# Kernel optimization log

Measured on AMD Instinct MI355X. Metric: run time of the kernel, lower is better.

Reference implementation:

```python
import jax, jax.numpy as jnp
import numpy as np

EPS = 1e-10  # faithful quirk: masked scores are set to eps, NOT -inf
LN_EPS = 1e-5
N_HEADS, D_MODEL, D_HEAD, D_MLP = 16, 1024, 64, 4096
INIT_RANGE = 0.02


def setup_inputs() -> dict:
    key = jax.random.key(0)
    ks = jax.random.split(key, 8)
    B, S = 2, 2048
    inp = {
        'residual': jax.random.normal(ks[0], (B, S, D_MODEL), jnp.float32),
        'W_key': jax.random.normal(ks[1], (N_HEADS, D_MODEL, D_HEAD), jnp.float32) * INIT_RANGE,
        'W_query': jax.random.normal(ks[2], (N_HEADS, D_MODEL, D_HEAD), jnp.float32) * INIT_RANGE,
        'W_values': jax.random.normal(ks[3], (N_HEADS, D_MODEL, D_HEAD), jnp.float32) * INIT_RANGE,
        'W_attn_out': jax.random.normal(ks[4], (N_HEADS, D_HEAD, D_MODEL), jnp.float32) * INIT_RANGE,
        'B_key': jnp.zeros((N_HEADS, D_HEAD), jnp.float32),
        'B_query': jnp.zeros((N_HEADS, D_HEAD), jnp.float32),
        'B_values': jnp.zeros((N_HEADS, D_HEAD), jnp.float32),
        'B_attn_out': jnp.zeros((D_MODEL,), jnp.float32),
        'ln1_w': jnp.ones((D_MODEL,), jnp.float32),
        'ln1_b': jnp.zeros((D_MODEL,), jnp.float32),
        'ln2_w': jnp.ones((D_MODEL,), jnp.float32),
        'ln2_b': jnp.zeros((D_MODEL,), jnp.float32),
        'W_mlp_in': jax.random.normal(ks[5], (D_MODEL, D_MLP), jnp.float32) * INIT_RANGE,
        'W_mlp_out': jax.random.normal(ks[6], (D_MLP, D_MODEL), jnp.float32) * INIT_RANGE,
        'B_mlp_in': jnp.zeros((D_MLP,), jnp.float32),
        'B_mlp_out': jnp.zeros((D_MODEL,), jnp.float32),
    }
    return inp


def _layernorm(x, w, b):
    mean = jnp.mean(x, axis=-1, keepdims=True)
    var = jnp.mean(jnp.square(x - mean), axis=-1, keepdims=True)  # biased var
    return (x - mean) / jnp.sqrt(var + LN_EPS) * w + b


def _attention(x, W_key, W_query, W_values, W_attn_out,
               B_key, B_query, B_values, B_attn_out):
    S = x.shape[1]
    keys = jnp.einsum('bse,neh->bsnh', x, W_key) + B_key
    queries = jnp.einsum('bse,neh->bsnh', x, W_query) + B_query
    values = jnp.einsum('bse,neh->bsnh', x, W_values) + B_values
    scores = jnp.einsum('bknh,bqnh->bnqk', keys, queries) / (D_HEAD ** 0.5)
    # faithful to source: positions where query < key are set to eps (not -inf)
    q_idx = jnp.arange(S)[:, None]
    k_idx = jnp.arange(S)[None, :]
    scores = jnp.where(q_idx < k_idx, EPS, scores)
    probs = jax.nn.softmax(scores, axis=3)
    weighted = jnp.einsum('bnqk,bknh->bqnh', probs, values)
    out = jnp.einsum('bqnh,nhe->bqe', weighted, W_attn_out) + B_attn_out
    return out


def reference(residual, W_key, W_query, W_values, W_attn_out,
              B_key, B_query, B_values, B_attn_out,
              ln1_w, ln1_b, ln2_w, ln2_b,
              W_mlp_in, W_mlp_out, B_mlp_in, B_mlp_out):
    mid = _attention(_layernorm(residual, ln1_w, ln1_b),
                     W_key, W_query, W_values, W_attn_out,
                     B_key, B_query, B_values, B_attn_out) + residual
    h = jnp.einsum('bse,em->bsm', _layernorm(mid, ln2_w, ln2_b), W_mlp_in) + B_mlp_in
    h = jax.nn.gelu(h, approximate=False)  # torch nn.GELU default = exact erf
    out = jnp.einsum('bsm,me->bse', h, W_mlp_out) + B_mlp_out + mid
    return out
```

## Files before the change

kernel.cpp:

```cpp
#include <hip/hip_runtime.h>
#include <hip/hip_bf16.h>


typedef __hip_bfloat16 bf16;
typedef __bf16 bf16x8 __attribute__((ext_vector_type(8)));
typedef float f32x4 __attribute__((ext_vector_type(4)));
typedef unsigned short u16x8 __attribute__((ext_vector_type(8)));
#define DEV static __device__ __forceinline__

DEV float b2f(bf16 v) { return __bfloat162float(v); }
DEV bf16 f2b(float v) { return __float2bfloat16(v); }
DEV unsigned short f2bu(float v) { return __builtin_bit_cast(unsigned short, __float2bfloat16(v)); }
DEV float ldin(const void* p, size_t i, int f32) {
  return f32 ? ((const float*)p)[i] : b2f(((const bf16*)p)[i]);
}
DEV void stout(void* p, size_t i, int f32, float v) {
  if (f32) ((float*)p)[i] = v;
  else     ((bf16*)p)[i] = f2b(v);
}
DEV f32x4 mfma16(bf16x8 a, bf16x8 b, f32x4 c) {
  return __builtin_amdgcn_mfma_f32_16x16x32_bf16(a, b, c, 0, 0, 0);
}
DEV float exp2fast(float x) {
  float r;
  asm volatile("v_exp_f32 %0, %1\n\ts_nop 0" : "=v"(r) : "v"(x));
  return r;
}
DEV void gload16(const void* g, void* l) {
  __builtin_amdgcn_global_load_lds(
      (const __attribute__((address_space(1))) unsigned int*)g,
      (__attribute__((address_space(3))) unsigned int*)l, 16, 0, 0);
}

__global__ void detect_kernel(const void* __restrict__ ln1w, int* __restrict__ flag) {
  if (threadIdx.x == 0 && blockIdx.x == 0) {
    const unsigned short* u = (const unsigned short*)ln1w;
    flag[0] = (u[0] == 0x3F80u) ? 0 : 1;
  }
}

__global__ void pack_bias(const void* __restrict__ Bq, const void* __restrict__ Bk,
                          const void* __restrict__ Bv, const void* __restrict__ Bao,
                          const void* __restrict__ Bmi, const void* __restrict__ Bmo,
                          const int* __restrict__ flagp, float* __restrict__ out) {
  int t = blockIdx.x * 256 + threadIdx.x;
  if (t >= 9216) return;
  int f32 = flagp[0];
  float v;
  if (t < 1024)      v = ldin(Bq, t, f32);
  else if (t < 2048) v = ldin(Bk, t - 1024, f32);
  else if (t < 3072) v = ldin(Bv, t - 2048, f32);
  else if (t < 4096) v = ldin(Bao, t - 3072, f32);
  else if (t < 8192) v = ldin(Bmi, t - 4096, f32);
  else               v = ldin(Bmo, t - 8192, f32);
  out[t] = v;
}

__global__ __launch_bounds__(256) void tsplit(const void* __restrict__ src,
                                              bf16* __restrict__ hi,
                                              const int* __restrict__ flagp,
                                              int K, int N) {
  int i = blockIdx.x * 256 + threadIdx.x;
  int f32 = flagp[0];
  int k = i / N, n = i - k * N;
  float v = ldin(src, i, f32);
  hi[(size_t)n * K + k] = f2b(v);
}

__global__ __launch_bounds__(256) void tsplit_qkv(const void* __restrict__ Wq,
                                                  const void* __restrict__ Wk,
                                                  const void* __restrict__ Wv,
                                                  bf16* __restrict__ hi,
                                                  const int* __restrict__ flagp) {
  int i = blockIdx.x * 256 + threadIdx.x;
  int f32 = flagp[0];
  int sec = i >> 20;
  int rem = i & 1048575;
  int hh = rem >> 16, kr = rem & 65535;
  int k = kr >> 6, d = kr & 63;
  const void* W = (sec == 0) ? Wq : (sec == 1) ? Wk : Wv;
  float v = ldin(W, (size_t)hh * 65536 + (size_t)k * 64 + d, f32);
  int n = sec * 1024 + hh * 64 + d;
  hi[(size_t)n * 1024 + k] = f2b(v);
}

__global__ __launch_bounds__(256) void vsuffix(const bf16* __restrict__ v2,
                                               float* __restrict__ suf) {
  const int head = blockIdx.x >> 6, d = blockIdx.x & 63;
  const int t = threadIdx.x;
  const int T = t >> 3, s0 = (t & 7) * 8;
  const bf16* src = v2 + (size_t)head * 131072 + (size_t)T * 4096 + d * 64 + s0;
  u16x8 u = *(const u16x8*)src;
  float s = 0.f;
#pragma unroll
  for (int j = 0; j < 8; j++) s += b2f(__builtin_bit_cast(bf16, (unsigned short)u[j]));
#pragma unroll
  for (int off = 1; off < 8; off <<= 1) s += __shfl_xor(s, off);
  __shared__ float cs[32];
  if ((t & 7) == 0) cs[T] = s;
  __syncthreads();
  if (t < 33) {
    float acc = 0.f;
    for (int j = t; j < 32; j++) acc += cs[j];
    suf[((size_t)head * 33 + t) * 64 + d] = acc;
  }
}

__global__ __launch_bounds__(256) void ln_kernel(const void* __restrict__ x,
                                                 const void* __restrict__ w,
                                                 const void* __restrict__ bb,
                                                 bf16* __restrict__ out,
                                                 const int* __restrict__ flagp) {
  const int f32 = flagp[0];
  const int row = blockIdx.x, t = threadIdx.x;
  const size_t base = (size_t)row * 1024;
  float v[4];
#pragma unroll
  for (int i = 0; i < 4; i++) v[i] = ldin(x, base + t + 256 * i, f32);
  float s1 = v[0] + v[1] + v[2] + v[3];
  float s2 = v[0] * v[0] + v[1] * v[1] + v[2] * v[2] + v[3] * v[3];
#pragma unroll
  for (int off = 32; off; off >>= 1) {
    s1 += __shfl_xor(s1, off);
    s2 += __shfl_xor(s2, off);
  }
  __shared__ float r1[4], r2[4];
  if ((t & 63) == 0) { r1[t >> 6] = s1; r2[t >> 6] = s2; }
  __syncthreads();
  s1 = r1[0] + r1[1] + r1[2] + r1[3];
  s2 = r2[0] + r2[1] + r2[2] + r2[3];
  float mean = s1 * (1.f / 1024.f);
  float var = s2 * (1.f / 1024.f) - mean * mean;
  float rstd = rsqrtf(var + 1e-5f);
#pragma unroll
  for (int i = 0; i < 4; i++) {
    int idx = t + 256 * i;
    out[base + idx] = f2b((v[i] - mean) * rstd * ldin(w, idx, f32) + ldin(bb, idx, f32));
  }
}

template <int MODE>
__global__ __launch_bounds__(256) void gemm_bt2(const bf16* __restrict__ A,
                                                const bf16* __restrict__ BT,
                                                const float* __restrict__ bias,
                                                const void* extra, void* outp,
                                                const int* __restrict__ flagp,
                                                int N, int K) {
  __shared__ __align__(16) unsigned short As[128][64];
  __shared__ __align__(16) unsigned short Bs[128][64];
  const int f32 = flagp[0];
  const int t = threadIdx.x;
  const int lane = t & 63, wv = t >> 6;
  const int quad = lane >> 4, l15 = lane & 15;
  const int wm = (wv >> 1) * 64, wn = (wv & 1) * 64;
  const int m0 = blockIdx.y * 128, n0 = blockIdx.x * 128;
  f32x4 acc[4][4] = {};
  const int rl = lane >> 3, G = lane & 7;
  const int sg = (G ^ rl) * 8;
  const int l7 = l15 & 7;
  for (int k0 = 0; k0 < K; k0 += 64) {
#pragma unroll
    for (int c = 0; c < 4; c++) {
      const int ch = wv * 4 + c;
      const int row = ch * 8 + rl;
      gload16(A + (size_t)(m0 + row) * K + k0 + sg, &As[ch * 8][0]);
      gload16(BT + (size_t)(n0 + row) * K + k0 + sg, &Bs[ch * 8][0]);
    }
    __syncthreads();
#pragma unroll
    for (int sub = 0; sub < 2; sub++) {
      const int gsw = (((sub * 4 + quad) ^ l7)) * 8;
      bf16x8 af[4], bh[4];
#pragma unroll
      for (int f = 0; f < 4; f++) {
        af[f] = __builtin_bit_cast(bf16x8, *(const u16x8*)&As[wm + f * 16 + l15][gsw]);
        bh[f] = __builtin_bit_cast(bf16x8, *(const u16x8*)&Bs[wn + f * 16 + l15][gsw]);
      }
#pragma unroll
      for (int fm = 0; fm < 4; fm++)
#pragma unroll
        for (int fn = 0; fn < 4; fn++)
          acc[fm][fn] = mfma16(af[fm], bh[fn], acc[fm][fn]);
    }
    __syncthreads();
  }
  if (MODE == 3) {
    bf16* q2 = (bf16*)outp;
    bf16* k2 = q2 + 4194304;
    bf16* v2 = (bf16*)const_cast<void*>(extra);
#pragma unroll
    for (int fm = 0; fm < 4; fm++) {
      int rowb = m0 + wm + fm * 16 + quad * 4;
      int bq = rowb >> 11, sb = rowb & 2047;
#pragma unroll
      for (int fn = 0; fn < 4; fn++) {
        int col = n0 + wn + fn * 16 + l15;
        float bcol = bias[col];
        int sec = col >> 10;
        int hd = col & 1023;
        size_t hbase = (size_t)(bq * 16 + (hd >> 6)) * 131072;
        int d = hd & 63;
        if (sec == 2) {
          unsigned long long pk = 0;
#pragma unroll
          for (int r = 0; r < 4; r++)
            pk |= (unsigned long long)f2bu(acc[fm][fn][r] + bcol) << (16 * r);
          *(unsigned long long*)&v2[hbase + (size_t)(sb >> 6) * 4096 + d * 64 + (sb & 63)] = pk;
        } else {
          bf16* dst = sec ? k2 : q2;
#pragma unroll
          for (int r = 0; r < 4; r++)
            dst[hbase + (size_t)(sb + r) * 64 + d] = f2b(acc[fm][fn][r] + bcol);
        }
      }
    }
  } else {
#pragma unroll
    for (int fm = 0; fm < 4; fm++) {
#pragma unroll
      for (int r = 0; r < 4; r++) {
        int row = m0 + wm + fm * 16 + quad * 4 + r;
#pragma unroll
        for (int fn = 0; fn < 4; fn++) {
          int col = n0 + wn + fn * 16 + l15;
          float v = acc[fm][fn][r] + bias[col];
          if (MODE == 1) {
            size_t idx = (size_t)row * N + col;
            v += ldin(extra, idx, f32);
            stout(outp, idx, f32, v);
          } else {
            v = 0.5f * v * (1.f + erff(v * 0.70710678118654752f));
            ((bf16*)outp)[(size_t)row * N + col] = f2b(v);
          }
        }
      }
    }
  }
}

__global__ __launch_bounds__(256) void gemm_bt3(const bf16* __restrict__ A,
                                                const bf16* __restrict__ BT,
                                                const float* __restrict__ bias,
                                                const void* extra, void* outp,
                                                const int* __restrict__ flagp,
                                                int N, int K) {
  __shared__ __align__(16) unsigned short As[64][64];
  __shared__ __align__(16) unsigned short Bs[128][64];
  const int f32 = flagp[0];
  const int t = threadIdx.x;
  const int lane = t & 63, wv = t >> 6;
  const int quad = lane >> 4, l15 = lane & 15;
  const int wm = (wv >> 1) * 32, wn = (wv & 1) * 64;
  const int m0 = blockIdx.y * 64, n0 = blockIdx.x * 128;
  f32x4 acc[2][4] = {};
  const int rl = lane >> 3, G = lane & 7;
  const int sg = (G ^ rl) * 8;
  const int l7 = l15 & 7;
  for (int k0 = 0; k0 < K; k0 += 64) {
#pragma unroll
    for (int c = 0; c < 2; c++) {
      const int ch = wv * 2 + c;
      gload16(A + (size_t)(m0 + ch * 8 + rl) * K + k0 + sg, &As[ch * 8][0]);
    }
#pragma unroll
    for (int c = 0; c < 4; c++) {
      const int ch = wv * 4 + c;
      gload16(BT + (size_t)(n0 + ch * 8 + rl) * K + k0 + sg, &Bs[ch * 8][0]);
    }
    __syncthreads();
#pragma unroll
    for (int sub = 0; sub < 2; sub++) {
      const int gsw = (((sub * 4 + quad) ^ l7)) * 8;
      bf16x8 af[2], bh[4];
#pragma unroll
      for (int f = 0; f < 2; f++)
        af[f] = __builtin_bit_cast(bf16x8, *(const u16x8*)&As[wm + f * 16 + l15][gsw]);
#pragma unroll
      for (int f = 0; f < 4; f++)
        bh[f] = __builtin_bit_cast(bf16x8, *(const u16x8*)&Bs[wn + f * 16 + l15][gsw]);
#pragma unroll
      for (int fm = 0; fm < 2; fm++)
#pragma unroll
        for (int fn = 0; fn < 4; fn++)
          acc[fm][fn] = mfma16(af[fm], bh[fn], acc[fm][fn]);
    }
    __syncthreads();
  }
#pragma unroll
  for (int fm = 0; fm < 2; fm++) {
#pragma unroll
    for (int r = 0; r < 4; r++) {
      int row = m0 + wm + fm * 16 + quad * 4 + r;
#pragma unroll
      for (int fn = 0; fn < 4; fn++) {
        int col = n0 + wn + fn * 16 + l15;
        float v = acc[fm][fn][r] + bias[col];
        size_t idx = (size_t)row * N + col;
        v += ldin(extra, idx, f32);
        stout(outp, idx, f32, v);
      }
    }
  }
}

template <int MODE, int QKV>
__global__ __launch_bounds__(256) void gemm_nn(const bf16* __restrict__ A,
                                               const void* __restrict__ B0,
                                               const void* __restrict__ B1,
                                               const void* __restrict__ B2,
                                               const float* __restrict__ bias,
                                               const void* extra, void* outp,
                                               const int* __restrict__ flagp,
                                               int N, int K, size_t ooff) {
  __shared__ unsigned short As[128][40];
  __shared__ unsigned short Bh[128][40];
  __shared__ unsigned short Bl[128][40];
  const int f32 = flagp[0];
  const int t = threadIdx.x;
  const int lane = t & 63, wv = t >> 6;
  const int quad = lane >> 4, l15 = lane & 15;
  const int wm = (wv >> 1) * 64, wn = (wv & 1) * 64;
  const int m0 = blockIdx.y * 128, n0 = blockIdx.x * 128;
  const void* B = B0;
  if (QKV) B = (n0 < 1024) ? B0 : (n0 < 2048) ? B1 : B2;
  f32x4 acc[4][4] = {};
  const int row_a = t >> 2;
  const int kc = (t & 3) * 8;
  const int cB = t & 127;
  const int e0 = t >> 7;
  for (int k0 = 0; k0 < K; k0 += 32) {
    uint4 a0 = *(const uint4*)(A + (size_t)(m0 + row_a) * K + k0 + kc);
    uint4 a1 = *(const uint4*)(A + (size_t)(m0 + 64 + row_a) * K + k0 + kc);
    *(uint4*)&As[row_a][kc] = a0;
    *(uint4*)&As[64 + row_a][kc] = a1;
#pragma unroll
    for (int rep = 0; rep < 8; rep++) {
      int e = (rep * 2 + e0) * 2;
      size_t a0i, a1i;
      if (QKV) {
        int cs = (n0 + cB) & 1023;
        size_t wb = (size_t)(cs >> 6) * 65536 + (cs & 63);
        a0i = wb + (size_t)(k0 + e) * 64;
        a1i = wb + (size_t)(k0 + e + 1) * 64;
      } else {
        a0i = (size_t)(k0 + e) * N + n0 + cB;
        a1i = a0i + N;
      }
      float v0 = ldin(B, a0i, f32);
      float v1 = ldin(B, a1i, f32);
      unsigned short h0 = f2bu(v0), h1 = f2bu(v1);
      float l0 = v0 - b2f(__builtin_bit_cast(bf16, h0));
      float l1 = v1 - b2f(__builtin_bit_cast(bf16, h1));
      *(unsigned int*)&Bh[cB][e] = (unsigned int)h0 | ((unsigned int)h1 << 16);
      *(unsigned int*)&Bl[cB][e] = (unsigned int)f2bu(l0) | ((unsigned int)f2bu(l1) << 16);
    }
    __syncthreads();
    bf16x8 af[4], bh[4], bl[4];
#pragma unroll
    for (int f = 0; f < 4; f++) {
      af[f] = __builtin_bit_cast(bf16x8, *(const u16x8*)&As[wm + f * 16 + l15][quad * 8]);
      bh[f] = __builtin_bit_cast(bf16x8, *(const u16x8*)&Bh[wn + f * 16 + l15][quad * 8]);
      bl[f] = __builtin_bit_cast(bf16x8, *(const u16x8*)&Bl[wn + f * 16 + l15][quad * 8]);
    }
#pragma unroll
    for (int fm = 0; fm < 4; fm++)
#pragma unroll
      for (int fn = 0; fn < 4; fn++)
        acc[fm][fn] = mfma16(af[fm], bh[fn], acc[fm][fn]);
    if (f32) {
#pragma unroll
      for (int fm = 0; fm < 4; fm++)
#pragma unroll
        for (int fn = 0; fn < 4; fn++)
          acc[fm][fn] = mfma16(af[fm], bl[fn], acc[fm][fn]);
    }
    __syncthreads();
  }
#pragma unroll
  for (int fm = 0; fm < 4; fm++) {
#pragma unroll
    for (int r = 0; r < 4; r++) {
      int row = m0 + wm + fm * 16 + quad * 4 + r;
#pragma unroll
      for (int fn = 0; fn < 4; fn++) {
        int col = n0 + wn + fn * 16 + l15;
        float v = acc[fm][fn][r] + bias[col];
        size_t idx = (size_t)row * N + col;
        if (MODE == 1) {
          v += ldin(extra, ooff + idx, f32);
          stout(outp, ooff + idx, f32, v);
        } else if (MODE == 2) {
          v = 0.5f * v * (1.f + erff(v * 0.70710678118654752f));
          ((bf16*)outp)[idx] = f2b(v);
        } else {
          ((bf16*)outp)[idx] = f2b(v);
        }
      }
    }
  }
}

__global__ __launch_bounds__(256) void attn_split(const bf16* __restrict__ qkv2,
                                                  const float* __restrict__ suf,
                                                  float* __restrict__ part0,
                                                  float* __restrict__ part1,
                                                  float* __restrict__ lp0buf,
                                                  float* __restrict__ lp1buf,
                                                  bf16* __restrict__ weighted) {
  __shared__ __align__(16) unsigned short P[2][4][16][72];
  const int t = threadIdx.x;
  const int lane = t & 63, wv = t >> 6;
  const int quad = lane >> 4, l15 = lane & 15;
  const int p = blockIdx.x;
  const int g = p & 31;
  const int wi = p >> 5;
  int qc, Tlo, Thi, mode;
  if (wi < 32) {
    qc = 31 - (wi >> 1);
    if ((wi & 1) == 0) { Tlo = 0; Thi = 15; mode = 1; }
    else               { Tlo = 16; Thi = qc; mode = 2; }
  } else {
    qc = 47 - wi; Tlo = 0; Thi = qc; mode = 0;
  }
  const int b = g >> 4, n = g & 15;
  const int q0 = qc * 64 + wv * 16;
  const bf16* Qh = qkv2 + (size_t)g * 131072;
  const bf16* Kh = qkv2 + 4194304 + (size_t)g * 131072;
  const bf16* Vh = qkv2 + 8388608 + (size_t)g * 131072;
  bf16x8 aq0, aq1;
  {
    u16x8 u0 = *(const u16x8*)(Qh + (size_t)(q0 + l15) * 64 + quad * 8);
    u16x8 u1 = *(const u16x8*)(Qh + (size_t)(q0 + l15) * 64 + 32 + quad * 8);
    aq0 = __builtin_bit_cast(bf16x8, u0);
    aq1 = __builtin_bit_cast(bf16x8, u1);
  }
  float lpA[4] = {0.f, 0.f, 0.f, 0.f}, lpB[4] = {0.f, 0.f, 0.f, 0.f};
  f32x4 oA[4] = {}, oB[4] = {};
  const float C = 0.125f * 1.44269504088896f;
  const int qgb = q0 + quad * 4;
  auto tile = [&](int T, int st, f32x4* o, float* lp) {
    const int kk = T * 64;
    const bf16* Vt = Vh + (size_t)T * 4096;
    u16x8 vu[2][4];
#pragma unroll
    for (int sl = 0; sl < 2; sl++)
#pragma unroll
      for (int f = 0; f < 4; f++)
        vu[sl][f] = *(const u16x8*)(Vt + (size_t)(f * 16 + l15) * 64 + sl * 32 + quad * 8);
    f32x4 s[4];
#pragma unroll
    for (int sub = 0; sub < 4; sub++) {
      int krow = kk + sub * 16 + l15;
      u16x8 uk0 = *(const u16x8*)(Kh + (size_t)krow * 64 + quad * 8);
      u16x8 uk1 = *(const u16x8*)(Kh + (size_t)krow * 64 + 32 + quad * 8);
      f32x4 sc = {0.f, 0.f, 0.f, 0.f};
      sc = mfma16(aq0, __builtin_bit_cast(bf16x8, uk0), sc);
      sc = mfma16(aq1, __builtin_bit_cast(bf16x8, uk1), sc);
      s[sub] = sc;
    }
#pragma unroll
    for (int sub = 0; sub < 4; sub++) {
#pragma unroll
      for (int r = 0; r < 4; r++) {
        float pv = exp2fast(s[sub][r] * C);
        int kg = kk + sub * 16 + l15;
        pv = (qgb + r < kg) ? 1.0f : pv;
        lp[r] += pv;
        P[st][wv][quad * 4 + r][l15 + 16 * sub] = f2bu(pv);
      }
    }
    u16x8 pu0 = *(const u16x8*)&P[st][wv][l15][quad * 8];
    u16x8 pu1 = *(const u16x8*)&P[st][wv][l15][32 + quad * 8];
#pragma unroll
    for (int f = 0; f < 4; f++) {
      o[f] = mfma16(__builtin_bit_cast(bf16x8, pu0), __builtin_bit_cast(bf16x8, vu[0][f]), o[f]);
      o[f] = mfma16(__builtin_bit_cast(bf16x8, pu1), __builtin_bit_cast(bf16x8, vu[1][f]), o[f]);
    }
  };
  int T = Tlo;
  for (; T + 1 <= Thi; T += 2) {
    tile(T, 0, oA, lpA);
    tile(T + 1, 1, oB, lpB);
  }
  if (T <= Thi) tile(T, 0, oA, lpA);
  float lp[4];
  f32x4 o[4];
#pragma unroll
  for (int r = 0; r < 4; r++) lp[r] = lpA[r] + lpB[r];
#pragma unroll
  for (int f = 0; f < 4; f++) o[f] = oA[f] + oB[f];
  if (mode != 1) {
    const float* sp = suf + ((size_t)g * 33 + (qc + 1)) * 64;
#pragma unroll
    for (int f = 0; f < 4; f++) {
      float sv = sp[f * 16 + l15];
#pragma unroll
      for (int r = 0; r < 4; r++) o[f][r] += sv;
    }
  }
#pragma unroll
  for (int off = 8; off; off >>= 1)
#pragma unroll
    for (int r = 0; r < 4; r++) lp[r] += __shfl_xor(lp[r], off);
  if (mode == 0) {
    const float mcnt = (float)(2048 - 64 * (qc + 1));
#pragma unroll
    for (int r = 0; r < 4; r++) {
      float inv = 1.f / (lp[r] + mcnt);
      int qg = q0 + quad * 4 + r;
      size_t base = (size_t)(b * 2048 + qg) * 1024 + n * 64;
#pragma unroll
      for (int f = 0; f < 4; f++)
        weighted[base + f * 16 + l15] = f2b(o[f][r] * inv);
    }
  } else {
    float* part = (mode == 1) ? part0 : part1;
    float* lpb  = (mode == 1) ? lp0buf : lp1buf;
    size_t pb = (size_t)(g * 16 + (qc - 16)) * 4096;
#pragma unroll
    for (int r = 0; r < 4; r++) {
      int row = wv * 16 + quad * 4 + r;
#pragma unroll
      for (int f = 0; f < 4; f++)
        part[pb + (size_t)row * 64 + f * 16 + l15] = o[f][r];
      if (l15 == 0) lpb[(size_t)(g * 16 + (qc - 16)) * 64 + row] = lp[r];
    }
  }
}

__global__ __launch_bounds__(256) void attn_combine(const float* __restrict__ part0,
                                                    const float* __restrict__ part1,
                                                    const float* __restrict__ lp0,
                                                    const float* __restrict__ lp1,
                                                    bf16* __restrict__ weighted) {
  int i = blockIdx.x * 256 + threadIdx.x;
  int d = i & 63, row = (i >> 6) & 63, qq = (i >> 12) & 15, g = i >> 16;
  int qc = qq + 16;
  size_t pi = ((size_t)(g * 16 + qq) * 64 + row) * 64 + d;
  float o = part0[pi] + part1[pi];
  size_t li = (size_t)(g * 16 + qq) * 64 + row;
  float mcnt = (float)(2048 - 64 * (qc + 1));
  float lp = lp0[li] + lp1[li] + mcnt;
  int b = g >> 4, n = g & 15;
  int qg = qc * 64 + row;
  weighted[(size_t)(b * 2048 + qg) * 1024 + n * 64 + d] = f2b(o / lp);
}

__global__ __launch_bounds__(256) void attn_old(const bf16* __restrict__ qkv,
                                                bf16* __restrict__ weighted) {
  __shared__ unsigned short P[4][16][40];
  const int t = threadIdx.x;
  const int lane = t & 63, wv = t >> 6;
  const int quad = lane >> 4, l15 = lane & 15;
  const int bid = blockIdx.x;
  const int qc = bid & 31, bn = bid >> 5;
  const int b = bn >> 4, n = bn & 15;
  const int q0 = qc * 64 + wv * 16;
  const bf16* Qb = qkv + (size_t)b * 2048 * 3072 + n * 64;
  const bf16* Kb = Qb + 1024;
  const unsigned short* Vus = (const unsigned short*)(Qb + 2048);
  bf16x8 aq0, aq1;
  {
    u16x8 u0 = *(const u16x8*)(Qb + (size_t)(q0 + l15) * 3072 + quad * 8);
    u16x8 u1 = *(const u16x8*)(Qb + (size_t)(q0 + l15) * 3072 + 32 + quad * 8);
    aq0 = __builtin_bit_cast(bf16x8, u0);
    aq1 = __builtin_bit_cast(bf16x8, u1);
  }
  float m_[4] = {-30000.f, -30000.f, -30000.f, -30000.f};
  float l_[4] = {0.f, 0.f, 0.f, 0.f};
  f32x4 o[4] = {};
  for (int kk = 0; kk < 2048; kk += 32) {
    f32x4 s[2];
#pragma unroll
    for (int sub = 0; sub < 2; sub++) {
      int krow = kk + sub * 16 + l15;
      u16x8 uk0 = *(const u16x8*)(Kb + (size_t)krow * 3072 + quad * 8);
      u16x8 uk1 = *(const u16x8*)(Kb + (size_t)krow * 3072 + 32 + quad * 8);
      f32x4 sc = {0.f, 0.f, 0.f, 0.f};
      sc = mfma16(aq0, __builtin_bit_cast(bf16x8, uk0), sc);
      sc = mfma16(aq1, __builtin_bit_cast(bf16x8, uk1), sc);
#pragma unroll
      for (int r = 0; r < 4; r++) {
        int qg = q0 + quad * 4 + r;
        int kg = kk + sub * 16 + l15;
        s[sub][r] = (qg < kg) ? 1e-10f : sc[r] * 0.125f;
      }
    }
    float mr[4];
#pragma unroll
    for (int r = 0; r < 4; r++) mr[r] = fmaxf(s[0][r], s[1][r]);
#pragma unroll
    for (int off = 8; off; off >>= 1)
#pragma unroll
      for (int r = 0; r < 4; r++) mr[r] = fmaxf(mr[r], __shfl_xor(mr[r], off));
    float al[4];
#pragma unroll
    for (int r = 0; r < 4; r++) {
      float mn = fmaxf(m_[r], mr[r]);
      al[r] = __expf(m_[r] - mn);
      m_[r] = mn;
    }
    f32x4 p0, p1;
    float rs[4];
#pragma unroll
    for (int r = 0; r < 4; r++) {
      p0[r] = __expf(s[0][r] - m_[r]);
      p1[r] = __expf(s[1][r] - m_[r]);
      rs[r] = p0[r] + p1[r];
    }
#pragma unroll
    for (int off = 8; off; off >>= 1)
#pragma unroll
      for (int r = 0; r < 4; r++) rs[r] += __shfl_xor(rs[r], off);
#pragma unroll
    for (int r = 0; r < 4; r++) l_[r] = l_[r] * al[r] + rs[r];
#pragma unroll
    for (int f = 0; f < 4; f++)
#pragma unroll
      for (int r = 0; r < 4; r++) o[f][r] *= al[r];
#pragma unroll
    for (int r = 0; r < 4; r++) {
      P[wv][quad * 4 + r][l15] = f2bu(p0[r]);
      P[wv][quad * 4 + r][16 + l15] = f2bu(p1[r]);
    }
    __syncthreads();
    u16x8 pu = *(const u16x8*)&P[wv][l15][quad * 8];
    bf16x8 pf = __builtin_bit_cast(bf16x8, pu);
#pragma unroll
    for (int f = 0; f < 4; f++) {
      u16x8 vu;
#pragma unroll
      for (int j = 0; j < 8; j++)
        vu[j] = Vus[(size_t)(kk + quad * 8 + j) * 3072 + f * 16 + l15];
      o[f] = mfma16(pf, __builtin_bit_cast(bf16x8, vu), o[f]);
    }
    __syncthreads();
  }
#pragma unroll
  for (int r = 0; r < 4; r++) {
    float inv = 1.f / l_[r];
    int qg = q0 + quad * 4 + r;
    size_t base = (size_t)(b * 2048 + qg) * 1024 + n * 64;
#pragma unroll
    for (int f = 0; f < 4; f++)
      weighted[base + f * 16 + l15] = f2b(o[f][r] * inv);
  }
}

extern "C" void kernel_launch(void* const* d_in, const int* in_sizes, int n_in,
                              void* d_out, int out_size, void* d_ws, size_t ws_size,
                              hipStream_t stream) {
  const void* residual = d_in[0];
  const void* W_key    = d_in[1];
  const void* W_query  = d_in[2];
  const void* W_values = d_in[3];
  const void* W_ao     = d_in[4];
  const void* B_key    = d_in[5];
  const void* B_query  = d_in[6];
  const void* B_values = d_in[7];
  const void* B_ao     = d_in[8];
  const void* ln1w     = d_in[9];
  const void* ln1b     = d_in[10];
  const void* ln2w     = d_in[11];
  const void* ln2b     = d_in[12];
  const void* W_mi     = d_in[13];
  const void* W_mo     = d_in[14];
  const void* B_mi     = d_in[15];
  const void* B_mo     = d_in[16];

  char* ws = (char*)d_ws;
  float* biasA  = (float*)ws;
  int*   flag   = (int*)(ws + 36864);
  bf16*  slotA  = (bf16*)(ws + 40960);
  bf16*  xn = slotA, *wtd = slotA, *xn2 = slotA;

  detect_kernel<<<1, 64, 0, stream>>>(ln1w, flag);
  pack_bias<<<36, 256, 0, stream>>>(B_query, B_key, B_values, B_ao, B_mi, B_mo,
                                    flag, biasA);

  if (ws_size >= (size_t)83927040) {
    bf16*  qkv2    = (bf16*)(ws + 8429568);
    bf16*  q2      = qkv2;
    bf16*  v2      = qkv2 + 8388608;
    bf16*  h       = (bf16*)(ws + 8429568);
    bf16*  qkvT_hi = (bf16*)(ws + 33595392);
    float* suf     = (float*)(ws + 39886848);
    float* lp0buf  = (float*)(ws + 40157184);
    float* lp1buf  = (float*)(ws + 40288256);
    bf16*  aoT_hi  = (bf16*)(ws + 46178304);
    bf16*  miT_hi  = (bf16*)(ws + 50372608);
    float* part0   = (float*)(ws + 58761216);
    bf16*  moT_hi  = (bf16*)(ws + 67149824);
    float* part1   = (float*)(ws + 75538432);

    tsplit_qkv<<<12288, 256, 0, stream>>>(W_query, W_key, W_values, qkvT_hi, flag);
    tsplit<<<4096, 256, 0, stream>>>(W_ao, aoT_hi, flag, 1024, 1024);
    tsplit<<<16384, 256, 0, stream>>>(W_mi, miT_hi, flag, 1024, 4096);
    tsplit<<<16384, 256, 0, stream>>>(W_mo, moT_hi, flag, 4096, 1024);

    ln_kernel<<<4096, 256, 0, stream>>>(residual, ln1w, ln1b, xn, flag);
    gemm_bt2<3><<<dim3(24, 32), 256, 0, stream>>>(xn, qkvT_hi, biasA,
                                                  v2, q2, flag, 3072, 1024);
    vsuffix<<<2048, 256, 0, stream>>>(v2, suf);
    attn_split<<<1536, 256, 0, stream>>>(qkv2, suf, part0, part1,
                                         lp0buf, lp1buf, wtd);
    attn_combine<<<8192, 256, 0, stream>>>(part0, part1, lp0buf, lp1buf, wtd);
    gemm_bt3<<<dim3(8, 64), 256, 0, stream>>>(wtd, aoT_hi, biasA + 3072,
                                              residual, d_out, flag, 1024, 1024);
    ln_kernel<<<4096, 256, 0, stream>>>(d_out, ln2w, ln2b, xn2, flag);
    gemm_bt2<2><<<dim3(32, 32), 256, 0, stream>>>(xn2, miT_hi, biasA + 4096,
                                                  nullptr, h, flag, 4096, 1024);
    gemm_bt3<<<dim3(8, 64), 256, 0, stream>>>(h, moT_hi, biasA + 8192,
                                              d_out, d_out, flag, 1024, 4096);
  } else {
    bf16* qkv   = (bf16*)(ws + 8429568);
    bf16* hhalf = (bf16*)(ws + 16818176);

    ln_kernel<<<4096, 256, 0, stream>>>(residual, ln1w, ln1b, xn, flag);
    gemm_nn<0, 1><<<dim3(24, 32), 256, 0, stream>>>(xn, W_query, W_key, W_values,
                                                    biasA, nullptr, qkv, flag,
                                                    3072, 1024, 0);
    attn_old<<<1024, 256, 0, stream>>>(qkv, wtd);
    gemm_nn<1, 0><<<dim3(8, 32), 256, 0, stream>>>(wtd, W_ao, nullptr, nullptr,
                                                   biasA + 3072, residual, d_out,
                                                   flag, 1024, 1024, 0);
    ln_kernel<<<4096, 256, 0, stream>>>(d_out, ln2w, ln2b, xn2, flag);
    for (int half = 0; half < 2; ++half) {
      const bf16* a2 = xn2 + (size_t)half * 2048 * 1024;
      size_t ooff = (size_t)half * 2048 * 1024;
      gemm_nn<2, 0><<<dim3(32, 16), 256, 0, stream>>>(a2, W_mi, nullptr, nullptr,
                                                      biasA + 4096, nullptr, hhalf,
                                                      flag, 4096, 1024, 0);
      gemm_nn<1, 0><<<dim3(8, 16), 256, 0, stream>>>(hhalf, W_mo, nullptr, nullptr,
                                                     biasA + 8192, d_out, d_out,
                                                     flag, 1024, 4096, ooff);
    }
  }
}
```

Measured before the change: 543.0 us.

## Give each attention wave a full 64-query chunk to reuse K/V loads

Each wavefront now handles all four 16-row query groups of a 64-query work item, where before the four waves of a block shared one item with 16 rows each. Every K/V tile a wave loads is reused across 64 queries, cutting redundant global and L2 traffic by roughly four times. The grid shrinks from 1536 to 384 blocks, and the even/odd double accumulators are dropped. The cost is many more live registers per wave (64 accumulator floats plus Q fragments), with launch_bounds(256,2) set to hold occupancy, and the total number of waves available to spread load imbalance falls.

```diff
diff --git a/kernel.cpp b/kernel.cpp
--- a/kernel.cpp
+++ b/kernel.cpp
@@ -400,20 +400,20 @@
   }
 }
 
-__global__ __launch_bounds__(256) void attn_split(const bf16* __restrict__ qkv2,
-                                                  const float* __restrict__ suf,
-                                                  float* __restrict__ part0,
-                                                  float* __restrict__ part1,
-                                                  float* __restrict__ lp0buf,
-                                                  float* __restrict__ lp1buf,
-                                                  bf16* __restrict__ weighted) {
-  __shared__ __align__(16) unsigned short P[2][4][16][72];
+__global__ __launch_bounds__(256, 2) void attn_split(const bf16* __restrict__ qkv2,
+                                                     const float* __restrict__ suf,
+                                                     float* __restrict__ part0,
+                                                     float* __restrict__ part1,
+                                                     float* __restrict__ lp0buf,
+                                                     float* __restrict__ lp1buf,
+                                                     bf16* __restrict__ weighted) {
+  __shared__ __align__(16) unsigned short P[4][4][16][72];
   const int t = threadIdx.x;
   const int lane = t & 63, wv = t >> 6;
   const int quad = lane >> 4, l15 = lane & 15;
-  const int p = blockIdx.x;
-  const int g = p & 31;
-  const int wi = p >> 5;
+  const int w = blockIdx.x * 4 + wv;
+  const int g = w & 31;
+  const int wi = w >> 5;
   int qc, Tlo, Thi, mode;
   if (wi < 32) {
     qc = 31 - (wi >> 1);
@@ -423,23 +423,28 @@
     qc = 47 - wi; Tlo = 0; Thi = qc; mode = 0;
   }
   const int b = g >> 4, n = g & 15;
-  const int q0 = qc * 64 + wv * 16;
   const bf16* Qh = qkv2 + (size_t)g * 131072;
   const bf16* Kh = qkv2 + 4194304 + (size_t)g * 131072;
   const bf16* Vh = qkv2 + 8388608 + (size_t)g * 131072;
-  bf16x8 aq0, aq1;
-  {
-    u16x8 u0 = *(const u16x8*)(Qh + (size_t)(q0 + l15) * 64 + quad * 8);
-    u16x8 u1 = *(const u16x8*)(Qh + (size_t)(q0 + l15) * 64 + 32 + quad * 8);
-    aq0 = __builtin_bit_cast(bf16x8, u0);
-    aq1 = __builtin_bit_cast(bf16x8, u1);
-  }
-  float lpA[4] = {0.f, 0.f, 0.f, 0.f}, lpB[4] = {0.f, 0.f, 0.f, 0.f};
-  f32x4 oA[4] = {}, oB[4] = {};
+  bf16x8 aq[4][2];
+#pragma unroll
+  for (int qg = 0; qg < 4; qg++) {
+    size_t qr = (size_t)(qc * 64 + qg * 16 + l15) * 64;
+    aq[qg][0] = __builtin_bit_cast(bf16x8, *(const u16x8*)(Qh + qr + quad * 8));
+    aq[qg][1] = __builtin_bit_cast(bf16x8, *(const u16x8*)(Qh + qr + 32 + quad * 8));
+  }
+  float lp[4][4] = {};
+  f32x4 o[4][4] = {};
   const float C = 0.125f * 1.44269504088896f;
-  const int qgb = q0 + quad * 4;
-  auto tile = [&](int T, int st, f32x4* o, float* lp) {
+  for (int T = Tlo; T <= Thi; ++T) {
     const int kk = T * 64;
+    u16x8 uk[4][2];
+#pragma unroll
+    for (int sub = 0; sub < 4; sub++) {
+      size_t kr = (size_t)(kk + sub * 16 + l15) * 64;
+      uk[sub][0] = *(const u16x8*)(Kh + kr + quad * 8);
+      uk[sub][1] = *(const u16x8*)(Kh + kr + 32 + quad * 8);
+    }
     const bf16* Vt = Vh + (size_t)T * 4096;
     u16x8 vu[2][4];
 #pragma unroll
@@ -447,83 +452,82 @@
 #pragma unroll
       for (int f = 0; f < 4; f++)
         vu[sl][f] = *(const u16x8*)(Vt + (size_t)(f * 16 + l15) * 64 + sl * 32 + quad * 8);
-    f32x4 s[4];
-#pragma unroll
-    for (int sub = 0; sub < 4; sub++) {
-      int krow = kk + sub * 16 + l15;
-      u16x8 uk0 = *(const u16x8*)(Kh + (size_t)krow * 64 + quad * 8);
-      u16x8 uk1 = *(const u16x8*)(Kh + (size_t)krow * 64 + 32 + quad * 8);
-      f32x4 sc = {0.f, 0.f, 0.f, 0.f};
-      sc = mfma16(aq0, __builtin_bit_cast(bf16x8, uk0), sc);
-      sc = mfma16(aq1, __builtin_bit_cast(bf16x8, uk1), sc);
-      s[sub] = sc;
-    }
-#pragma unroll
-    for (int sub = 0; sub < 4; sub++) {
-#pragma unroll
-      for (int r = 0; r < 4; r++) {
-        float pv = exp2fast(s[sub][r] * C);
-        int kg = kk + sub * 16 + l15;
-        pv = (qgb + r < kg) ? 1.0f : pv;
-        lp[r] += pv;
-        P[st][wv][quad * 4 + r][l15 + 16 * sub] = f2bu(pv);
-      }
-    }
-    u16x8 pu0 = *(const u16x8*)&P[st][wv][l15][quad * 8];
-    u16x8 pu1 = *(const u16x8*)&P[st][wv][l15][32 + quad * 8];
-#pragma unroll
-    for (int f = 0; f < 4; f++) {
-      o[f] = mfma16(__builtin_bit_cast(bf16x8, pu0), __builtin_bit_cast(bf16x8, vu[0][f]), o[f]);
-      o[f] = mfma16(__builtin_bit_cast(bf16x8, pu1), __builtin_bit_cast(bf16x8, vu[1][f]), o[f]);
-    }
-  };
-  int T = Tlo;
-  for (; T + 1 <= Thi; T += 2) {
-    tile(T, 0, oA, lpA);
-    tile(T + 1, 1, oB, lpB);
-  }
-  if (T <= Thi) tile(T, 0, oA, lpA);
-  float lp[4];
-  f32x4 o[4];
-#pragma unroll
-  for (int r = 0; r < 4; r++) lp[r] = lpA[r] + lpB[r];
-#pragma unroll
-  for (int f = 0; f < 4; f++) o[f] = oA[f] + oB[f];
+#pragma unroll
+    for (int qg = 0; qg < 4; qg++) {
+      const int qgb = qc * 64 + qg * 16 + quad * 4;
+      f32x4 s[4];
+#pragma unroll
+      for (int sub = 0; sub < 4; sub++) {
+        f32x4 sc = {0.f, 0.f, 0.f, 0.f};
+        sc = mfma16(aq[qg][0], __builtin_bit_cast(bf16x8, uk[sub][0]), sc);
+        sc = mfma16(aq[qg][1], __builtin_bit_cast(bf16x8, uk[sub][1]), sc);
+        s[sub] = sc;
+      }
+#pragma unroll
+      for (int sub = 0; sub < 4; sub++) {
+#pragma unroll
+        for (int r = 0; r < 4; r++) {
+          float pv = exp2fast(s[sub][r] * C);
+          int kg = kk + sub * 16 + l15;
+          pv = (qgb + r < kg) ? 1.0f : pv;
+          lp[qg][r] += pv;
+          P[wv][qg][quad * 4 + r][l15 + 16 * sub] = f2bu(pv);
+        }
+      }
+      u16x8 pu0 = *(const u16x8*)&P[wv][qg][l15][quad * 8];
+      u16x8 pu1 = *(const u16x8*)&P[wv][qg][l15][32 + quad * 8];
+#pragma unroll
+      for (int f = 0; f < 4; f++) {
+        o[qg][f] = mfma16(__builtin_bit_cast(bf16x8, pu0), __builtin_bit_cast(bf16x8, vu[0][f]), o[qg][f]);
+        o[qg][f] = mfma16(__builtin_bit_cast(bf16x8, pu1), __builtin_bit_cast(bf16x8, vu[1][f]), o[qg][f]);
+      }
+    }
+  }
   if (mode != 1) {
     const float* sp = suf + ((size_t)g * 33 + (qc + 1)) * 64;
 #pragma unroll
     for (int f = 0; f < 4; f++) {
       float sv = sp[f * 16 + l15];
 #pragma unroll
-      for (int r = 0; r < 4; r++) o[f][r] += sv;
+      for (int qg = 0; qg < 4; qg++)
+#pragma unroll
+        for (int r = 0; r < 4; r++) o[qg][f][r] += sv;
     }
   }
 #pragma unroll
   for (int off = 8; off; off >>= 1)
 #pragma unroll
-    for (int r = 0; r < 4; r++) lp[r] += __shfl_xor(lp[r], off);
+    for (int qg = 0; qg < 4; qg++)
+#pragma unroll
+      for (int r = 0; r < 4; r++) lp[qg][r] += __shfl_xor(lp[qg][r], off);
   if (mode == 0) {
     const float mcnt = (float)(2048 - 64 * (qc + 1));
 #pragma unroll
-    for (int r = 0; r < 4; r++) {
-      float inv = 1.f / (lp[r] + mcnt);
-      int qg = q0 + quad * 4 + r;
-      size_t base = (size_t)(b * 2048 + qg) * 1024 + n * 64;
-#pragma unroll
-      for (int f = 0; f < 4; f++)
-        weighted[base + f * 16 + l15] = f2b(o[f][r] * inv);
+    for (int qg = 0; qg < 4; qg++) {
+#pragma unroll
+      for (int r = 0; r < 4; r++) {
+        float inv = 1.f / (lp[qg][r] + mcnt);
+        int qg_row = qc * 64 + qg * 16 + quad * 4 + r;
+        size_t base = (size_t)(b * 2048 + qg_row) * 1024 + n * 64;
+#pragma unroll
+        for (int f = 0; f < 4; f++)
+          weighted[base + f * 16 + l15] = f2b(o[qg][f][r] * inv);
+      }
     }
   } else {
     float* part = (mode == 1) ? part0 : part1;
     float* lpb  = (mode == 1) ? lp0buf : lp1buf;
     size_t pb = (size_t)(g * 16 + (qc - 16)) * 4096;
 #pragma unroll
-    for (int r = 0; r < 4; r++) {
-      int row = wv * 16 + quad * 4 + r;
-#pragma unroll
-      for (int f = 0; f < 4; f++)
-        part[pb + (size_t)row * 64 + f * 16 + l15] = o[f][r];
-      if (l15 == 0) lpb[(size_t)(g * 16 + (qc - 16)) * 64 + row] = lp[r];
+    for (int qg = 0; qg < 4; qg++) {
+#pragma unroll
+      for (int r = 0; r < 4; r++) {
+        int row = qg * 16 + quad * 4 + r;
+#pragma unroll
+        for (int f = 0; f < 4; f++)
+          part[pb + (size_t)row * 64 + f * 16 + l15] = o[qg][f][r];
+        if (l15 == 0) lpb[(size_t)(g * 16 + (qc - 16)) * 64 + row] = lp[qg][r];
+      }
     }
   }
 }
@@ -702,8 +706,8 @@
     gemm_bt2<3><<<dim3(24, 32), 256, 0, stream>>>(xn, qkvT_hi, biasA,
                                                   v2, q2, flag, 3072, 1024);
     vsuffix<<<2048, 256, 0, stream>>>(v2, suf);
-    attn_split<<<1536, 256, 0, stream>>>(qkv2, suf, part0, part1,
-                                         lp0buf, lp1buf, wtd);
+    attn_split<<<384, 256, 0, stream>>>(qkv2, suf, part0, part1,
+                                        lp0buf, lp1buf, wtd);
     attn_combine<<<8192, 256, 0, stream>>>(part0, part1, lp0buf, lp1buf, wtd);
     gemm_bt3<<<dim3(8, 64), 256, 0, stream>>>(wtd, aoT_hi, biasA + 3072,
                                               residual, d_out, flag, 1024, 1024);
```

After: 465.3 us. 14.3% less time.
